# Optimization experiments

Hardware: AMD Instinct MI355X
Metric: run time of the kernel (lower is better)

Reference implementation:

```python
import jax, jax.numpy as jnp
import numpy as np

B, H, S, D = 4, 16, 2048, 64

def setup_inputs() -> dict:
    key = jax.random.key(0)
    kq, kk, kv = jax.random.split(key, 3)
    return {
        "query": jax.random.normal(kq, (B, H, S, D), dtype=jnp.float32),
        "key": jax.random.normal(kk, (B, H, S, D), dtype=jnp.float32),
        "value": jax.random.normal(kv, (B, H, S, D), dtype=jnp.float32),
        "dropout_p": 0,
    }

def reference(query, key, value, dropout_p):
    # qk: [B,H,S,S] materialized as in the original (unfused SDPA)
    scale = query.shape[-1] ** -0.5
    qk = jnp.einsum("bhqd,bhkd->bhqk", query, key) * scale
    attn = jax.nn.softmax(qk, axis=-1)
    # dropout_p == 0 -> identity (keeps reference deterministic)
    out = jnp.einsum("bhqk,bhkd->bhqd", attn, value)
    return out
```

## Files before the change

kernel.cpp:

```cpp
#include <hip/hip_runtime.h>
#include <hip/hip_bf16.h>

#define B_   4
#define H_   16
#define SEQ  2048
#define DH   64
#define BM   128
#define BN   64
#define NBH  (B_ * H_)
#define NELEM (NBH * SEQ * DH)

typedef __bf16 bf16x8 __attribute__((ext_vector_type(8)));
typedef float  f32x4  __attribute__((ext_vector_type(4)));
typedef float  f32x16 __attribute__((ext_vector_type(16)));
typedef unsigned short u16x8 __attribute__((ext_vector_type(8)));
typedef unsigned short u16x4 __attribute__((ext_vector_type(4)));

__device__ __forceinline__ unsigned short f2bu(float x) {
    __hip_bfloat16 h = __float2bfloat16(x);
    return __builtin_bit_cast(unsigned short, h);
}

__device__ __forceinline__ void ld_lds16(const unsigned short* g, unsigned short* l) {
    __builtin_amdgcn_global_load_lds(
        (const __attribute__((address_space(1))) unsigned int*)(g),
        (__attribute__((address_space(3))) unsigned int*)(l), 16, 0, 0);
}

__global__ __launch_bounds__(256)
void prep_kv(const float* __restrict__ K, const float* __restrict__ V,
             unsigned short* __restrict__ Kb, unsigned short* __restrict__ Vt) {
    __shared__ unsigned short tile[64 * 72];
    const int bh = blockIdx.y;
    const int s0 = blockIdx.x * 64;
    const int t  = threadIdx.x;

    {
        const float* Ki = K + (size_t)bh * SEQ * DH + (size_t)s0 * DH;
        unsigned short* Ko = Kb + (size_t)bh * SEQ * DH + (size_t)s0 * DH;
        for (int jj = 0; jj < 2; ++jj) {
            const int e = (jj * 256 + t) * 8;
            const float4 a = *reinterpret_cast<const float4*>(Ki + e);
            const float4 b = *reinterpret_cast<const float4*>(Ki + e + 4);
            u16x8 u;
            u[0] = f2bu(a.x); u[1] = f2bu(a.y); u[2] = f2bu(a.z); u[3] = f2bu(a.w);
            u[4] = f2bu(b.x); u[5] = f2bu(b.y); u[6] = f2bu(b.z); u[7] = f2bu(b.w);
            *reinterpret_cast<u16x8*>(Ko + e) = u;
        }
    }

    const float* Vb = V + (size_t)bh * SEQ * DH + (size_t)s0 * DH;
    unsigned short* Vo = Vt + (size_t)bh * DH * SEQ;
    {
        const int sl = t >> 2, d0 = (t & 3) * 16;
        for (int c = 0; c < 4; ++c) {
            const float4 v = *reinterpret_cast<const float4*>(Vb + sl * DH + d0 + c * 4);
            u16x4 u; u[0] = f2bu(v.x); u[1] = f2bu(v.y); u[2] = f2bu(v.z); u[3] = f2bu(v.w);
            *reinterpret_cast<u16x4*>(&tile[sl * 72 + d0 + c * 4]) = u;
        }
    }
    __syncthreads();
    {
        const int d = t >> 2, sc0 = (t & 3) * 16;
        for (int c = 0; c < 2; ++c) {
            const int s = sc0 + c * 8;
            u16x8 u;
#pragma unroll
            for (int r = 0; r < 8; ++r) u[r] = tile[(s + r) * 72 + d];
            *reinterpret_cast<u16x8*>(Vo + (size_t)d * SEQ + s0 + s) = u;
        }
    }
}

__global__ __launch_bounds__(256, 3)
void fa_fwd(const float* __restrict__ Qg, const unsigned short* __restrict__ Kb,
            const unsigned short* __restrict__ Vtb, float* __restrict__ Og)
{
    __shared__ __attribute__((aligned(16))) unsigned short smem[16384];

    const int tid  = threadIdx.x;
    const int lane = tid & 63;
    const int wave = tid >> 6;
    const int l31  = lane & 31;
    const int hi   = lane >> 5;

    const int bid   = blockIdx.x;
    const int xcd   = bid & 7;
    const int jj    = bid >> 3;
    const int bh    = (xcd << 3) | (jj >> 4);
    const int qtile = jj & 15;

    const float*          Qb  = Qg  + (size_t)bh * SEQ * DH;
    const unsigned short* Kbh = Kb  + (size_t)bh * SEQ * DH;
    const unsigned short* Vbh = Vtb + (size_t)bh * DH * SEQ;
    float*                Ob  = Og  + (size_t)bh * SEQ * DH;

    const int qrow0 = qtile * BM + wave * 32;

    const float CS = 0.125f * 1.4426950408889634f;

    bf16x8 Qf[4];
#pragma unroll
    for (int kt = 0; kt < 4; ++kt) {
        const float* qsrc = Qb + (size_t)(qrow0 + l31) * DH + kt * 16 + hi * 8;
        const float4 a = *reinterpret_cast<const float4*>(qsrc);
        const float4 b = *reinterpret_cast<const float4*>(qsrc + 4);
        union { bf16x8 v; unsigned short u[8]; } tmp;
        tmp.u[0] = f2bu(a.x * CS); tmp.u[1] = f2bu(a.y * CS);
        tmp.u[2] = f2bu(a.z * CS); tmp.u[3] = f2bu(a.w * CS);
        tmp.u[4] = f2bu(b.x * CS); tmp.u[5] = f2bu(b.y * CS);
        tmp.u[6] = f2bu(b.z * CS); tmp.u[7] = f2bu(b.w * CS);
        Qf[kt] = tmp.v;
    }

    const f32x16 z16 = {0.f,0.f,0.f,0.f, 0.f,0.f,0.f,0.f,
                        0.f,0.f,0.f,0.f, 0.f,0.f,0.f,0.f};

    f32x16 OA = z16, OB = z16;
    float Lp0 = 0.f, Lp1 = 0.f;

    const unsigned short* kp[2];
    const unsigned short* vp[2];
    int koff_st[2], voff_st[2];
    for (int i = 0; i < 2; ++i) {
        const int beta = i * 256 + tid;
        {
            const int s    = beta >> 3;
            const int b    = beta & 7;
            const int gnat = b ^ ((s & 7) ^ ((s >> 3) & 7));
            const int grow = (s & 3) + 4 * ((s >> 3) & 1) + 8 * ((s >> 2) & 1)
                           + 16 * ((s >> 4) & 1) + 32 * (s >> 5);
            kp[i]  = Kbh + (size_t)grow * DH + gnat * 8;
        }
        {
            const int d = beta >> 3;
            const int g = (beta & 7) ^ ((d & 7) ^ ((d >> 3) & 7));
            vp[i]  = Vbh + (size_t)d * SEQ + g * 8;
        }
        koff_st[i] = (i * 256 + wave * 64) * 8;
        voff_st[i] = 4096 + (i * 256 + wave * 64) * 8;
    }

    const int kA = (l31 & 7) ^ ((l31 >> 3) & 7);
    int rdA[4], rdB[4];
#pragma unroll
    for (int c = 0; c < 4; ++c) {
        rdA[c] = l31 * 64 + (((((c << 1) | hi)) ^ kA) << 3);
        rdB[c] = rdA[c] ^ 32;
    }

#define STAGE(BUF) do {                                                        \
        _Pragma("unroll")                                                      \
        for (int i = 0; i < 2; ++i) {                                          \
            ld_lds16(kp[i], smem + (BUF) * 8192 + koff_st[i]);                 \
            kp[i] += BN * DH;                                                  \
        }                                                                      \
        _Pragma("unroll")                                                      \
        for (int i = 0; i < 2; ++i) {                                          \
            ld_lds16(vp[i], smem + (BUF) * 8192 + voff_st[i]);                 \
            vp[i] += BN;                                                       \
        }                                                                      \
    } while (0)

#define QK_TILE(BUF, T, S, RD) do {                                            \
        _Pragma("unroll")                                                      \
        for (int kt = 0; kt < 4; ++kt) {                                       \
            const bf16x8 kf = *reinterpret_cast<const bf16x8*>(                \
                &smem[(BUF) * 8192 + (T) * 2048 + RD[kt]]);                    \
            S = __builtin_amdgcn_mfma_f32_32x32x16_bf16(kf, Qf[kt],            \
                    (kt == 0) ? z16 : S, 0, 0, 0);                             \
        }                                                                      \
    } while (0)

#define SM_TILE(S, T) do {                                                     \
        float p[16];                                                           \
        _Pragma("unroll")                                                      \
        for (int r = 0; r < 16; ++r) p[r] = __builtin_amdgcn_exp2f(S[r]);      \
        _Pragma("unroll")                                                      \
        for (int c1 = 0; c1 < 2; ++c1) {                                       \
            union { bf16x8 v; unsigned w[4]; } a;                              \
            _Pragma("unroll")                                                  \
            for (int w = 0; w < 4; ++w) {                                      \
                const unsigned u0 = __builtin_bit_cast(unsigned, p[8*c1 + 2*w    ]) + 0x8000u; \
                const unsigned u1 = __builtin_bit_cast(unsigned, p[8*c1 + 2*w + 1]) + 0x8000u; \
                a.w[w] = __builtin_amdgcn_perm(u1, u0, 0x07060302u);           \
            }                                                                  \
            af[2 * (T) + c1] = a.v;                                            \
        }                                                                      \
        _Pragma("unroll")                                                      \
        for (int r = 0; r < 8; ++r)  Lp0 += p[r];                              \
        _Pragma("unroll")                                                      \
        for (int r = 8; r < 16; ++r) Lp1 += p[r];                              \
    } while (0)

#define PV_ALL(BUF) do {                                                       \
        _Pragma("unroll")                                                      \
        for (int m = 0; m < 4; ++m) {                                          \
            const bf16x8 bv0 = *reinterpret_cast<const bf16x8*>(               \
                &smem[(BUF) * 8192 + 4096 + rdA[m]]);                          \
            const bf16x8 bv1 = *reinterpret_cast<const bf16x8*>(               \
                &smem[(BUF) * 8192 + 4096 + 2048 + rdB[m]]);                   \
            OA = __builtin_amdgcn_mfma_f32_32x32x16_bf16(af[m], bv0, OA, 0, 0, 0); \
            OB = __builtin_amdgcn_mfma_f32_32x32x16_bf16(af[m], bv1, OB, 0, 0, 0); \
        }                                                                      \
    } while (0)

#define COMPUTE(BUF) do {                                                      \
        bf16x8 af[4];                                                          \
        f32x16 S;                                                              \
        __builtin_amdgcn_s_setprio(1);                                         \
        QK_TILE(BUF, 0, S, rdA);                                               \
        __builtin_amdgcn_s_setprio(0);                                         \
        SM_TILE(S, 0);                                                         \
        __builtin_amdgcn_s_setprio(1);                                         \
        QK_TILE(BUF, 1, S, rdB);                                               \
        __builtin_amdgcn_s_setprio(0);                                         \
        SM_TILE(S, 1);                                                         \
        __builtin_amdgcn_s_setprio(1);                                         \
        PV_ALL(BUF);                                                           \
        __builtin_amdgcn_s_setprio(0);                                         \
    } while (0)

    STAGE(0);
    __syncthreads();

#pragma unroll 1
    for (int it2 = 0; it2 < 15; ++it2) {
        STAGE(1);
        COMPUTE(0);
        __syncthreads();
        STAGE(0);
        COMPUTE(1);
        __syncthreads();
    }
    STAGE(1);
    COMPUTE(0);
    __syncthreads();
    COMPUTE(1);

#undef STAGE
#undef QK_TILE
#undef SM_TILE
#undef PV_ALL
#undef COMPUTE

    float Lsum = Lp0 + Lp1;
    Lsum += __shfl_xor(Lsum, 32, 64);
    const float invq = 1.0f / Lsum;
    const int hi16 = hi << 4;

#pragma unroll
    for (int r = 0; r < 16; ++r) {
        const int qb = (r & 3) + 8 * (r >> 2);
        const float invr = __builtin_bit_cast(float,
            __builtin_amdgcn_ds_bpermute((qb << 2) + hi16,
                                         __builtin_bit_cast(int, invq)));
        const int row = qrow0 + qb + 4 * hi;
        float* orow = Ob + (size_t)row * DH + l31;
        orow[0]  = OA[r] * invr;
        orow[32] = OB[r] * invr;
    }
}

extern "C" void kernel_launch(void* const* d_in, const int* in_sizes, int n_in,
                              void* d_out, int out_size, void* d_ws, size_t ws_size,
                              hipStream_t stream) {
    const float* Q = (const float*)d_in[0];
    const float* K = (const float*)d_in[1];
    const float* V = (const float*)d_in[2];
    float* O = (float*)d_out;

    unsigned short* Kb = (unsigned short*)d_ws;
    unsigned short* Vt = Kb + (size_t)NELEM;

    prep_kv<<<dim3(SEQ / 64, NBH), 256, 0, stream>>>(K, V, Kb, Vt);
    fa_fwd<<<dim3((SEQ / BM) * NBH), dim3(256), 0, stream>>>(Q, Kb, Vt, O);
}
```

Measured before the change: 205.9 us.

## Software-pipeline QK and softmax across tiles with triple-buffered LDS

Moves from double to triple buffering of K/V tiles in shared memory and restructures the loop so each step computes the next QK tile before running softmax and the PV MFMAs for the previous one. Softmax exp work is interleaved with independent MFMAs, which is meant to hide the transcendental and conversion latency behind matrix ops. It also drops the setprio hints. The cost is 48KB of LDS per block instead of 32KB, which could limit occupancy, plus more live registers for two S accumulators.

```diff
diff --git a/kernel.cpp b/kernel.cpp
--- a/kernel.cpp
+++ b/kernel.cpp
@@ -76,7 +76,7 @@
 void fa_fwd(const float* __restrict__ Qg, const unsigned short* __restrict__ Kb,
             const unsigned short* __restrict__ Vtb, float* __restrict__ Og)
 {
-    __shared__ __attribute__((aligned(16))) unsigned short smem[16384];
+    __shared__ __attribute__((aligned(16))) unsigned short smem[24576];
 
     const int tid  = threadIdx.x;
     const int lane = tid & 63;
@@ -172,7 +172,7 @@
         }                                                                      \
     } while (0)
 
-#define SM_TILE(S, T) do {                                                     \
+#define SM_C(S, AF) do {                                                       \
         float p[16];                                                           \
         _Pragma("unroll")                                                      \
         for (int r = 0; r < 16; ++r) p[r] = __builtin_amdgcn_exp2f(S[r]);      \
@@ -185,7 +185,7 @@
                 const unsigned u1 = __builtin_bit_cast(unsigned, p[8*c1 + 2*w + 1]) + 0x8000u; \
                 a.w[w] = __builtin_amdgcn_perm(u1, u0, 0x07060302u);           \
             }                                                                  \
-            af[2 * (T) + c1] = a.v;                                            \
+            AF[c1] = a.v;                                                      \
         }                                                                      \
         _Pragma("unroll")                                                      \
         for (int r = 0; r < 8; ++r)  Lp0 += p[r];                              \
@@ -193,56 +193,56 @@
         for (int r = 8; r < 16; ++r) Lp1 += p[r];                              \
     } while (0)
 
-#define PV_ALL(BUF) do {                                                       \
-        _Pragma("unroll")                                                      \
-        for (int m = 0; m < 4; ++m) {                                          \
+#define PV_HALF(BUF, T, AF) do {                                               \
+        _Pragma("unroll")                                                      \
+        for (int mm = 0; mm < 2; ++mm) {                                       \
+            const int m = 2 * (T) + mm;                                        \
             const bf16x8 bv0 = *reinterpret_cast<const bf16x8*>(               \
                 &smem[(BUF) * 8192 + 4096 + rdA[m]]);                          \
             const bf16x8 bv1 = *reinterpret_cast<const bf16x8*>(               \
                 &smem[(BUF) * 8192 + 4096 + 2048 + rdB[m]]);                   \
-            OA = __builtin_amdgcn_mfma_f32_32x32x16_bf16(af[m], bv0, OA, 0, 0, 0); \
-            OB = __builtin_amdgcn_mfma_f32_32x32x16_bf16(af[m], bv1, OB, 0, 0, 0); \
-        }                                                                      \
-    } while (0)
-
-#define COMPUTE(BUF) do {                                                      \
-        bf16x8 af[4];                                                          \
-        f32x16 S;                                                              \
-        __builtin_amdgcn_s_setprio(1);                                         \
-        QK_TILE(BUF, 0, S, rdA);                                               \
-        __builtin_amdgcn_s_setprio(0);                                         \
-        SM_TILE(S, 0);                                                         \
-        __builtin_amdgcn_s_setprio(1);                                         \
-        QK_TILE(BUF, 1, S, rdB);                                               \
-        __builtin_amdgcn_s_setprio(0);                                         \
-        SM_TILE(S, 1);                                                         \
-        __builtin_amdgcn_s_setprio(1);                                         \
-        PV_ALL(BUF);                                                           \
-        __builtin_amdgcn_s_setprio(0);                                         \
-    } while (0)
+            OA = __builtin_amdgcn_mfma_f32_32x32x16_bf16(AF[mm], bv0, OA, 0, 0, 0); \
+            OB = __builtin_amdgcn_mfma_f32_32x32x16_bf16(AF[mm], bv1, OB, 0, 0, 0); \
+        }                                                                      \
+    } while (0)
+
+#define STEP(B0, B1, B2) do {                                                  \
+        STAGE(B2);                                                             \
+        QK_TILE(B0, 1, SB, rdB);               \
+        { bf16x8 af2[2]; SM_C(SA, af2); PV_HALF(B0, 0, af2); }  \
+        QK_TILE(B1, 0, SA, rdA);                  \
+        { bf16x8 af2[2]; SM_C(SB, af2); PV_HALF(B0, 1, af2); }  \
+        __syncthreads();                                                       \
+    } while (0)
+
+    f32x16 SA, SB;
 
     STAGE(0);
     __syncthreads();
+    STAGE(1);
+    QK_TILE(0, 0, SA, rdA);
+    __syncthreads();
 
 #pragma unroll 1
-    for (int it2 = 0; it2 < 15; ++it2) {
-        STAGE(1);
-        COMPUTE(0);
-        __syncthreads();
-        STAGE(0);
-        COMPUTE(1);
-        __syncthreads();
-    }
-    STAGE(1);
-    COMPUTE(0);
-    __syncthreads();
-    COMPUTE(1);
+    for (int it3 = 0; it3 < 10; ++it3) {
+        STEP(0, 1, 2);
+        STEP(1, 2, 0);
+        STEP(2, 0, 1);
+    }
+
+    QK_TILE(0, 1, SB, rdB);
+    { bf16x8 af2[2]; SM_C(SA, af2); PV_HALF(0, 0, af2); }
+    QK_TILE(1, 0, SA, rdA);
+    { bf16x8 af2[2]; SM_C(SB, af2); PV_HALF(0, 1, af2); }
+    QK_TILE(1, 1, SB, rdB);
+    { bf16x8 af2[2]; SM_C(SA, af2); PV_HALF(1, 0, af2); }
+    { bf16x8 af2[2]; SM_C(SB, af2); PV_HALF(1, 1, af2); }
 
 #undef STAGE
 #undef QK_TILE
-#undef SM_TILE
-#undef PV_ALL
-#undef COMPUTE
+#undef SM_C
+#undef PV_HALF
+#undef STEP
 
     float Lsum = Lp0 + Lp1;
     Lsum += __shfl_xor(Lsum, 32, 64);
```

After: 204.9 us. Within noise of the previous version (-0.5%).
